# Kernel tuning notes

Measured on AMD Instinct MI355X. Metric: run time of the kernel, lower is better.

Reference implementation:

```python
import jax, jax.numpy as jnp
import numpy as np

HEAD_DIM = 64
HIDDEN_SIZE = 3072
NUM_HEADS = 48
B, TXT, VID = 1, 256, 1792
N = TXT + VID


def _layernorm(x, g, b, eps=1e-5):
    mu = jnp.mean(x, axis=-1, keepdims=True)
    xc = x - mu
    var = jnp.mean(xc * xc, axis=-1, keepdims=True)
    return xc * jax.lax.rsqrt(var + eps) * g + b


def _apply_rope1(x, freqs):
    # x: [B, L, H, D]; freqs: [1, 1, Lf, D//2, 2, 2]
    Bx, L, H, D = x.shape
    x_ = x.reshape(Bx, L, H, D // 2, 1, 2)
    # faithful to torch: if dim-2 sizes mismatch (H vs Lf), slice freqs to H
    if x_.shape[2] != 1 and freqs.shape[2] != 1 and x_.shape[2] != freqs.shape[2]:
        freqs = freqs[:, :, : x_.shape[2]]
    out = freqs[..., 0] * x_[..., 0] + freqs[..., 1] * x_[..., 1]
    return out.reshape(Bx, L, H, D).astype(x.dtype)


def setup_inputs() -> dict:
    key = jax.random.key(0)
    ks = jax.random.split(key, 16)
    s = 1.0 / np.sqrt(HIDDEN_SIZE)
    d = dict(
        combined=jax.random.normal(ks[0], (B, N, HIDDEN_SIZE), jnp.float32),
        freqs=jax.random.normal(ks[1], (1, 1, VID, HEAD_DIM // 2, 2, 2), jnp.float32),
        Wq=jax.random.normal(ks[2], (HIDDEN_SIZE, HIDDEN_SIZE), jnp.float32) * s,
        bq=jnp.zeros((HIDDEN_SIZE,), jnp.float32),
        Wk=jax.random.normal(ks[3], (HIDDEN_SIZE, HIDDEN_SIZE), jnp.float32) * s,
        bk=jnp.zeros((HIDDEN_SIZE,), jnp.float32),
        Wv=jax.random.normal(ks[4], (HIDDEN_SIZE, HIDDEN_SIZE), jnp.float32) * s,
        bv=jnp.zeros((HIDDEN_SIZE,), jnp.float32),
        Wo=jax.random.normal(ks[5], (HIDDEN_SIZE, HIDDEN_SIZE), jnp.float32) * s,
        bo=jnp.zeros((HIDDEN_SIZE,), jnp.float32),
        gq=jnp.ones((HEAD_DIM,), jnp.float32),
        bgq=jnp.zeros((HEAD_DIM,), jnp.float32),
        gk=jnp.ones((HEAD_DIM,), jnp.float32),
        bgk=jnp.zeros((HEAD_DIM,), jnp.float32),
        txt_len=TXT,
    )
    return d


def reference(combined, freqs, Wq, bq, Wk, bk, Wv, bv, Wo, bo, gq, bgq, gk, bgk, txt_len):
    Bx, Nx, _ = combined.shape
    Q = (combined @ Wq.T + bq).reshape(Bx, Nx, NUM_HEADS, HEAD_DIM)
    K = (combined @ Wk.T + bk).reshape(Bx, Nx, NUM_HEADS, HEAD_DIM)
    V = (combined @ Wv.T + bv).reshape(Bx, Nx, NUM_HEADS, HEAD_DIM)
    Q = _layernorm(Q, gq, bgq)
    K = _layernorm(K, gk, bgk)
    if freqs is not None and Nx - txt_len > 0:
        Q_vid = _apply_rope1(Q[:, txt_len:], freqs)
        K_vid = _apply_rope1(K[:, txt_len:], freqs)
        Q = jnp.concatenate([Q[:, :txt_len], Q_vid], axis=1)
        K = jnp.concatenate([K[:, :txt_len], K_vid], axis=1)
    # SDPA in fp32: [B, H, N, D]
    q = Q.transpose(0, 2, 1, 3).astype(jnp.float32)
    k = K.transpose(0, 2, 1, 3).astype(jnp.float32)
    v = V.transpose(0, 2, 1, 3).astype(jnp.float32)
    scale = 1.0 / np.sqrt(HEAD_DIM)
    scores = jnp.einsum('bhqd,bhkd->bhqk', q, k) * scale
    probs = jax.nn.softmax(scores, axis=-1)
    attn = jnp.einsum('bhqk,bhkd->bhqd', probs, v).astype(combined.dtype)
    attn = attn.transpose(0, 2, 1, 3).reshape(Bx, Nx, HIDDEN_SIZE)
    out = attn @ Wo.T + bo
    return out[:, txt_len:], out[:, :txt_len]
```

## Files before the change

kernel.cpp:

```cpp
#include <hip/hip_runtime.h>
#include <hip/hip_bf16.h>

typedef __attribute__((ext_vector_type(8))) short bf16x8;
typedef __attribute__((ext_vector_type(4))) float f32x4;
typedef unsigned int __attribute__((address_space(1))) as1_uint;
typedef unsigned int __attribute__((address_space(3))) as3_uint;

#define TXT 256
#define VIDN 1792
#define SEQ 2048
#define HID 3072
#define NH 48
#define HD 64
#define QSCALE 0.18033688011112042f

__device__ __forceinline__ unsigned short f2bf(float f) {
  union { float f; unsigned int u; } x; x.f = f;
  unsigned int r = x.u + 0x7fffu + ((x.u >> 16) & 1u);
  return (unsigned short)(r >> 16);
}

__device__ __forceinline__ void gload16(const void* g, void* l) {
  __builtin_amdgcn_global_load_lds((const as1_uint*)g, (as3_uint*)l, 16, 0, 0);
}

__global__ __launch_bounds__(256) void cvt_kernel(const float* __restrict__ s,
                                                  unsigned short* __restrict__ d, int n) {
  int i = (blockIdx.x * 256 + threadIdx.x) * 4;
  if (i >= n) return;
  float4 v = *(const float4*)(s + i);
  ushort4 o;
  o.x = f2bf(v.x); o.y = f2bf(v.y); o.z = f2bf(v.z); o.w = f2bf(v.w);
  *(ushort4*)(d + i) = o;
}

__global__ __launch_bounds__(256) void cvt3_kernel(const float* __restrict__ a,
                                                   const float* __restrict__ b,
                                                   const float* __restrict__ c,
                                                   unsigned short* __restrict__ d) {
  const int per = (HID * HID) / 1024;
  int bid = blockIdx.x;
  int m = bid / per, r = bid - m * per;
  const float* s = (m == 0) ? a : (m == 1) ? b : c;
  int i = (r * 256 + threadIdx.x) * 4;
  float4 v = *(const float4*)(s + i);
  ushort4 o;
  o.x = f2bf(v.x); o.y = f2bf(v.y); o.z = f2bf(v.z); o.w = f2bf(v.w);
  *(ushort4*)(d + (size_t)m * HID * HID + i) = o;
}

template<int MODE>
__global__ __launch_bounds__(512) void gemm256(
    const unsigned short* __restrict__ A,
    const unsigned short* __restrict__ Bt,
    int K, int ntn,
    float* __restrict__ Cq, unsigned short* __restrict__ Vt, const float* __restrict__ bv,
    float* __restrict__ Cout, const float* __restrict__ bo)
{
  __shared__ unsigned short lds[4 * 2 * 8192];
  const int tid = threadIdx.x;
  const int mt = blockIdx.x / ntn, nt = blockIdx.x % ntn;
  const int m0 = mt * 256, n0 = nt * 256;
  const int w = tid >> 6, lane = tid & 63, lr = lane & 15, lg = lane >> 4;
  const int wr = w >> 2, wc = w & 3;
  f32x4 acc[8][4] = {};
  const int NT = K >> 5;

#define STAGE(t)                                                               \
  {                                                                            \
    const int slot_ = (t) & 3;                                                 \
    const int k0_ = (t) << 5;                                                  \
    _Pragma("unroll")                                                          \
    for (int c = 0; c < 2; ++c) {                                              \
      int off = (c * 512 + tid) * 16;                                          \
      int row = off >> 6, cb = off & 63;                                       \
      gload16(A + (size_t)(m0 + row) * K + k0_ + (cb >> 1),                    \
              (char*)lds + slot_ * 32768 + off);                               \
      gload16(Bt + (size_t)(n0 + row) * K + k0_ + (cb >> 1),                   \
              (char*)lds + slot_ * 32768 + 16384 + off);                       \
    }                                                                          \
  }

#define COMPUTE(t)                                                             \
  {                                                                            \
    const unsigned short* lA = lds + ((t) & 3) * 16384;                        \
    const unsigned short* lB = lA + 8192;                                      \
    bf16x8 bfr[4];                                                             \
    _Pragma("unroll")                                                          \
    for (int nf = 0; nf < 4; ++nf)                                             \
      bfr[nf] = *(const bf16x8*)&lB[(wc * 64 + nf * 16 + lr) * 32 + lg * 8];   \
    __builtin_amdgcn_s_setprio(1);                                             \
    _Pragma("unroll")                                                          \
    for (int mf = 0; mf < 8; ++mf) {                                           \
      bf16x8 af = *(const bf16x8*)&lA[(wr * 128 + mf * 16 + lr) * 32 + lg * 8];\
      acc[mf][0] = __builtin_amdgcn_mfma_f32_16x16x32_bf16(af, bfr[0], acc[mf][0], 0, 0, 0); \
      acc[mf][1] = __builtin_amdgcn_mfma_f32_16x16x32_bf16(af, bfr[1], acc[mf][1], 0, 0, 0); \
      acc[mf][2] = __builtin_amdgcn_mfma_f32_16x16x32_bf16(af, bfr[2], acc[mf][2], 0, 0, 0); \
      acc[mf][3] = __builtin_amdgcn_mfma_f32_16x16x32_bf16(af, bfr[3], acc[mf][3], 0, 0, 0); \
    }                                                                          \
    __builtin_amdgcn_s_setprio(0);                                             \
  }

  STAGE(0); STAGE(1); STAGE(2);
  int t = 0;
  for (; t < NT - 3; ++t) {
    __builtin_amdgcn_s_barrier();
    STAGE(t + 3);
    asm volatile("s_waitcnt vmcnt(12)" ::: "memory");
    COMPUTE(t);
  }
  __builtin_amdgcn_s_barrier();
  asm volatile("s_waitcnt vmcnt(8)" ::: "memory");
  COMPUTE(t); ++t;
  __builtin_amdgcn_s_barrier();
  asm volatile("s_waitcnt vmcnt(4)" ::: "memory");
  COMPUTE(t); ++t;
  __builtin_amdgcn_s_barrier();
  asm volatile("s_waitcnt vmcnt(0)" ::: "memory");
  COMPUTE(t);
#undef STAGE
#undef COMPUTE

  if (MODE == 0) {
    if (n0 < 6144) {
#pragma unroll
      for (int mf = 0; mf < 8; ++mf) {
        int row = m0 + wr * 128 + mf * 16 + lg * 4;
#pragma unroll
        for (int nf = 0; nf < 4; ++nf) {
          int col = n0 + wc * 64 + nf * 16 + lr;
#pragma unroll
          for (int j = 0; j < 4; ++j)
            Cq[(size_t)(row + j) * 6144 + col] = acc[mf][nf][j];
        }
      }
    } else {
#pragma unroll
      for (int mf = 0; mf < 8; ++mf) {
        int srow = m0 + wr * 128 + mf * 16 + lg * 4;
#pragma unroll
        for (int nf = 0; nf < 4; ++nf) {
          int n2 = n0 - 6144 + wc * 64 + nf * 16 + lr;
          float b = bv[n2];
          ushort4 pk;
          pk.x = f2bf(acc[mf][nf][0] + b);
          pk.y = f2bf(acc[mf][nf][1] + b);
          pk.z = f2bf(acc[mf][nf][2] + b);
          pk.w = f2bf(acc[mf][nf][3] + b);
          *(ushort4*)(Vt + (size_t)n2 * SEQ + srow) = pk;
        }
      }
    }
  } else {
#pragma unroll
    for (int mf = 0; mf < 8; ++mf) {
      int row = m0 + wr * 128 + mf * 16 + lg * 4;
#pragma unroll
      for (int nf = 0; nf < 4; ++nf) {
        int col = n0 + wc * 64 + nf * 16 + lr;
        float b = bo[col];
#pragma unroll
        for (int j = 0; j < 4; ++j) {
          int s = row + j;
          int orow = (s >= TXT) ? (s - TXT) : (VIDN + s);
          Cout[(size_t)orow * HID + col] = acc[mf][nf][j] + b;
        }
      }
    }
  }
}

__global__ __launch_bounds__(256) void ln_rope_kernel(
    const float* __restrict__ QK,
    const float* __restrict__ bq, const float* __restrict__ bk,
    const float* __restrict__ gq, const float* __restrict__ bgq,
    const float* __restrict__ gk, const float* __restrict__ bgk,
    const float* __restrict__ freqs,
    unsigned short* __restrict__ Qh, unsigned short* __restrict__ Kh)
{
  int wid = blockIdx.x * 4 + (threadIdx.x >> 6);
  int lane = threadIdx.x & 63;
  int s = wid / 96;
  int rem = wid - s * 96;
  int h = rem >> 1, qk = rem & 1;
  int col = h * 64 + lane;
  float x = QK[(size_t)s * 6144 + qk * 3072 + col] + (qk ? bk[col] : bq[col]);
  float m = x;
#pragma unroll
  for (int msk = 1; msk < 64; msk <<= 1) m += __shfl_xor(m, msk);
  float mu = m * (1.0f / 64.0f);
  float xc = x - mu;
  float v = xc * xc;
#pragma unroll
  for (int msk = 1; msk < 64; msk <<= 1) v += __shfl_xor(v, msk);
  float rstd = rsqrtf(v * (1.0f / 64.0f) + 1e-5f);
  float y = xc * rstd * (qk ? gk[lane] : gq[lane]) + (qk ? bgk[lane] : bgq[lane]);
  if (s >= TXT) {
    float p = __shfl_xor(y, 1);
    float xe = (lane & 1) ? p : y;
    float xo = (lane & 1) ? y : p;
    int base = h * 128 + (lane >> 1) * 4 + (lane & 1) * 2;
    y = freqs[base] * xe + freqs[base + 1] * xo;
  }
  if (!qk) y *= QSCALE;
  (qk ? Kh : Qh)[((size_t)h * SEQ + s) * 64 + lane] = f2bf(y);
}

__global__ __launch_bounds__(512) void fattn_kernel(
    const unsigned short* __restrict__ Qh, const unsigned short* __restrict__ Kh,
    const unsigned short* __restrict__ Vt, unsigned short* __restrict__ ctx)
{
  __shared__ unsigned short kt[2][64][32];
  __shared__ unsigned short vt[2][64][32];
  __shared__ unsigned short pl[8][16][72];
  const int h = blockIdx.x >> 4;
  const int q0 = (blockIdx.x & 15) * 128;
  const int tid = threadIdx.x, w = tid >> 6, lane = tid & 63, lr = lane & 15, lg = lane >> 4;

  bf16x8 qf0, qf1;
  {
    const unsigned short* qp = Qh + ((size_t)h * SEQ + q0 + w * 16 + lr) * 64 + lg * 8;
    qf0 = *(const bf16x8*)qp;
    qf1 = *(const bf16x8*)(qp + 32);
  }
  f32x4 oacc[4] = {};
  float mrun = -1e30f, lrun = 0.f;

  for (int kv0 = 0; kv0 < SEQ; kv0 += 64) {
    __syncthreads();
    {
      int off = tid * 16;
      int half = off >> 12;
      int rem = off & 4095;
      int row = rem >> 6, cb = rem & 63;
      gload16(Kh + ((size_t)h * SEQ + kv0 + row) * 64 + half * 32 + (cb >> 1), (char*)kt + off);
      gload16(Vt + ((size_t)(h * 64 + row)) * SEQ + kv0 + half * 32 + (cb >> 1), (char*)vt + off);
    }
    __syncthreads();

    f32x4 sacc[4] = {};
    __builtin_amdgcn_s_setprio(1);
#pragma unroll
    for (int nf = 0; nf < 4; ++nf) {
      bf16x8 a0 = *(const bf16x8*)&kt[0][nf * 16 + lr][lg * 8];
      bf16x8 a1 = *(const bf16x8*)&kt[1][nf * 16 + lr][lg * 8];
      sacc[nf] = __builtin_amdgcn_mfma_f32_16x16x32_bf16(a0, qf0, sacc[nf], 0, 0, 0);
      sacc[nf] = __builtin_amdgcn_mfma_f32_16x16x32_bf16(a1, qf1, sacc[nf], 0, 0, 0);
    }
    __builtin_amdgcn_s_setprio(0);

    float mx;
    {
      float t0 = fmaxf(fmaxf(sacc[0][0], sacc[0][1]), fmaxf(sacc[0][2], sacc[0][3]));
      float t1 = fmaxf(fmaxf(sacc[1][0], sacc[1][1]), fmaxf(sacc[1][2], sacc[1][3]));
      float t2 = fmaxf(fmaxf(sacc[2][0], sacc[2][1]), fmaxf(sacc[2][2], sacc[2][3]));
      float t3 = fmaxf(fmaxf(sacc[3][0], sacc[3][1]), fmaxf(sacc[3][2], sacc[3][3]));
      mx = fmaxf(fmaxf(t0, t1), fmaxf(t2, t3));
    }
    mx = fmaxf(mx, __shfl_xor(mx, 16));
    mx = fmaxf(mx, __shfl_xor(mx, 32));

    if (!__all(mx <= mrun + 8.0f)) {
      float mn = fmaxf(mrun, mx);
      float corr = exp2f(mrun - mn);
      lrun *= corr;
      mrun = mn;
      float c0 = __shfl(corr, lg * 4 + 0);
      float c1 = __shfl(corr, lg * 4 + 1);
      float c2 = __shfl(corr, lg * 4 + 2);
      float c3 = __shfl(corr, lg * 4 + 3);
#pragma unroll
      for (int df = 0; df < 4; ++df) {
        oacc[df][0] *= c0; oacc[df][1] *= c1;
        oacc[df][2] *= c2; oacc[df][3] *= c3;
      }
    }

    float pr[4][4];
#pragma unroll
    for (int nf = 0; nf < 4; ++nf)
#pragma unroll
      for (int r = 0; r < 4; ++r)
        pr[nf][r] = exp2f(sacc[nf][r] - mrun);
    float rs;
    {
      float s0 = (pr[0][0] + pr[0][1]) + (pr[0][2] + pr[0][3]);
      float s1 = (pr[1][0] + pr[1][1]) + (pr[1][2] + pr[1][3]);
      float s2 = (pr[2][0] + pr[2][1]) + (pr[2][2] + pr[2][3]);
      float s3 = (pr[3][0] + pr[3][1]) + (pr[3][2] + pr[3][3]);
      rs = (s0 + s1) + (s2 + s3);
    }
    rs += __shfl_xor(rs, 16);
    rs += __shfl_xor(rs, 32);
    lrun += rs;

#pragma unroll
    for (int nf = 0; nf < 4; ++nf) {
      union { __hip_bfloat162 h; unsigned int u; } c0, c1;
      c0.h = __float22bfloat162_rn(make_float2(pr[nf][0], pr[nf][1]));
      c1.h = __float22bfloat162_rn(make_float2(pr[nf][2], pr[nf][3]));
      uint2 pw; pw.x = c0.u; pw.y = c1.u;
      *(uint2*)&pl[w][lr][nf * 16 + lg * 4] = pw;
    }

    bf16x8 pa0 = *(const bf16x8*)&pl[w][lr][lg * 8];
    bf16x8 pa1 = *(const bf16x8*)&pl[w][lr][32 + lg * 8];
    __builtin_amdgcn_s_setprio(1);
#pragma unroll
    for (int df = 0; df < 4; ++df) {
      bf16x8 v0 = *(const bf16x8*)&vt[0][df * 16 + lr][lg * 8];
      bf16x8 v1 = *(const bf16x8*)&vt[1][df * 16 + lr][lg * 8];
      oacc[df] = __builtin_amdgcn_mfma_f32_16x16x32_bf16(pa0, v0, oacc[df], 0, 0, 0);
      oacc[df] = __builtin_amdgcn_mfma_f32_16x16x32_bf16(pa1, v1, oacc[df], 0, 0, 0);
    }
    __builtin_amdgcn_s_setprio(0);
  }

  float linv = 1.0f / lrun;
  float i0 = __shfl(linv, lg * 4 + 0);
  float i1 = __shfl(linv, lg * 4 + 1);
  float i2 = __shfl(linv, lg * 4 + 2);
  float i3 = __shfl(linv, lg * 4 + 3);
#pragma unroll
  for (int df = 0; df < 4; ++df) {
    int s = q0 + w * 16 + lg * 4;
    int dcol = h * 64 + df * 16 + lr;
    ctx[(size_t)(s + 0) * HID + dcol] = f2bf(oacc[df][0] * i0);
    ctx[(size_t)(s + 1) * HID + dcol] = f2bf(oacc[df][1] * i1);
    ctx[(size_t)(s + 2) * HID + dcol] = f2bf(oacc[df][2] * i2);
    ctx[(size_t)(s + 3) * HID + dcol] = f2bf(oacc[df][3] * i3);
  }
}

extern "C" void kernel_launch(void* const* d_in, const int* in_sizes, int n_in,
                              void* d_out, int out_size, void* d_ws, size_t ws_size,
                              hipStream_t stream) {
  const float* combined = (const float*)d_in[0];
  const float* freqs    = (const float*)d_in[1];
  const float* Wq  = (const float*)d_in[2];
  const float* bq  = (const float*)d_in[3];
  const float* Wk  = (const float*)d_in[4];
  const float* bk  = (const float*)d_in[5];
  const float* Wv  = (const float*)d_in[6];
  const float* bv  = (const float*)d_in[7];
  const float* Wo  = (const float*)d_in[8];
  const float* bo  = (const float*)d_in[9];
  const float* gq  = (const float*)d_in[10];
  const float* bgq = (const float*)d_in[11];
  const float* gk  = (const float*)d_in[12];
  const float* bgk = (const float*)d_in[13];
  float* out = (float*)d_out;

  char* ws = (char*)d_ws;
  unsigned short* Abf  = (unsigned short*)ws; ws += (size_t)SEQ * HID * 2;
  unsigned short* Wqkv = (unsigned short*)ws; ws += (size_t)3 * HID * HID * 2;
  float*          QK   = (float*)ws;          ws += (size_t)SEQ * 6144 * 4;
  unsigned short* Qh   = (unsigned short*)ws; ws += (size_t)NH * SEQ * HD * 2;
  unsigned short* Kh   = (unsigned short*)ws; ws += (size_t)NH * SEQ * HD * 2;
  unsigned short* Vt   = (unsigned short*)ws; ws += (size_t)NH * HD * SEQ * 2;
  unsigned short* Wob  = (unsigned short*)QK;
  unsigned short* ctx  = Abf;

  cvt_kernel<<<(SEQ * HID) / 1024, 256, 0, stream>>>(combined, Abf, SEQ * HID);
  cvt3_kernel<<<3 * (HID * HID) / 1024, 256, 0, stream>>>(Wq, Wk, Wv, Wqkv);

  gemm256<0><<<8 * 36, 512, 0, stream>>>(Abf, Wqkv, HID, 36, QK, Vt, bv, nullptr, nullptr);

  ln_rope_kernel<<<(SEQ * NH * 2) / 4, 256, 0, stream>>>(QK, bq, bk, gq, bgq, gk, bgk, freqs, Qh, Kh);

  cvt_kernel<<<(HID * HID) / 1024, 256, 0, stream>>>(Wo, Wob, HID * HID);

  fattn_kernel<<<NH * 16, 512, 0, stream>>>(Qh, Kh, Vt, ctx);

  gemm256<1><<<8 * 12, 512, 0, stream>>>(ctx, Wob, HID, 12, nullptr, nullptr, nullptr, out, bo);
}
```

Baseline: 453.7 us.

## Shrink GEMM M-tile to 128 and use 3-stage LDS pipeline for more blocks

Measured after the change: 430.2 us. 5.2% less time.

```diff
diff --git a/kernel.cpp b/kernel.cpp
--- a/kernel.cpp
+++ b/kernel.cpp
@@ -22,6 +22,12 @@
 
 __device__ __forceinline__ void gload16(const void* g, void* l) {
   __builtin_amdgcn_global_load_lds((const as1_uint*)g, (as3_uint*)l, 16, 0, 0);
+}
+
+__device__ __forceinline__ void fbar() {
+  asm volatile("" ::: "memory");
+  __builtin_amdgcn_s_barrier();
+  asm volatile("" ::: "memory");
 }
 
 __global__ __launch_bounds__(256) void cvt_kernel(const float* __restrict__ s,
@@ -50,49 +56,53 @@
 }
 
 template<int MODE>
-__global__ __launch_bounds__(512) void gemm256(
+__global__ __launch_bounds__(512, 4) void gemm256(
     const unsigned short* __restrict__ A,
     const unsigned short* __restrict__ Bt,
     int K, int ntn,
     float* __restrict__ Cq, unsigned short* __restrict__ Vt, const float* __restrict__ bv,
     float* __restrict__ Cout, const float* __restrict__ bo)
 {
-  __shared__ unsigned short lds[4 * 2 * 8192];
+  __shared__ unsigned short lds[3 * 12288];
   const int tid = threadIdx.x;
   const int mt = blockIdx.x / ntn, nt = blockIdx.x % ntn;
-  const int m0 = mt * 256, n0 = nt * 256;
+  const int m0 = mt * 128, n0 = nt * 256;
   const int w = tid >> 6, lane = tid & 63, lr = lane & 15, lg = lane >> 4;
   const int wr = w >> 2, wc = w & 3;
-  f32x4 acc[8][4] = {};
+  f32x4 acc[4][4] = {};
   const int NT = K >> 5;
 
 #define STAGE(t)                                                               \
   {                                                                            \
-    const int slot_ = (t) & 3;                                                 \
+    const int slot_ = (t) % 3;                                                 \
     const int k0_ = (t) << 5;                                                  \
+    char* base_ = (char*)lds + slot_ * 24576;                                  \
+    {                                                                          \
+      int off = tid * 16;                                                      \
+      int row = off >> 6, cb = off & 63;                                       \
+      gload16(A + (size_t)(m0 + row) * K + k0_ + (cb >> 1), base_ + off);      \
+    }                                                                          \
     _Pragma("unroll")                                                          \
     for (int c = 0; c < 2; ++c) {                                              \
       int off = (c * 512 + tid) * 16;                                          \
       int row = off >> 6, cb = off & 63;                                       \
-      gload16(A + (size_t)(m0 + row) * K + k0_ + (cb >> 1),                    \
-              (char*)lds + slot_ * 32768 + off);                               \
       gload16(Bt + (size_t)(n0 + row) * K + k0_ + (cb >> 1),                   \
-              (char*)lds + slot_ * 32768 + 16384 + off);                       \
+              base_ + 8192 + off);                                             \
     }                                                                          \
   }
 
 #define COMPUTE(t)                                                             \
   {                                                                            \
-    const unsigned short* lA = lds + ((t) & 3) * 16384;                        \
-    const unsigned short* lB = lA + 8192;                                      \
+    const unsigned short* lA = lds + ((t) % 3) * 12288;                        \
+    const unsigned short* lB = lA + 4096;                                      \
     bf16x8 bfr[4];                                                             \
     _Pragma("unroll")                                                          \
     for (int nf = 0; nf < 4; ++nf)                                             \
       bfr[nf] = *(const bf16x8*)&lB[(wc * 64 + nf * 16 + lr) * 32 + lg * 8];   \
     __builtin_amdgcn_s_setprio(1);                                             \
     _Pragma("unroll")                                                          \
-    for (int mf = 0; mf < 8; ++mf) {                                           \
-      bf16x8 af = *(const bf16x8*)&lA[(wr * 128 + mf * 16 + lr) * 32 + lg * 8];\
+    for (int mf = 0; mf < 4; ++mf) {                                           \
+      bf16x8 af = *(const bf16x8*)&lA[(wr * 64 + mf * 16 + lr) * 32 + lg * 8]; \
       acc[mf][0] = __builtin_amdgcn_mfma_f32_16x16x32_bf16(af, bfr[0], acc[mf][0], 0, 0, 0); \
       acc[mf][1] = __builtin_amdgcn_mfma_f32_16x16x32_bf16(af, bfr[1], acc[mf][1], 0, 0, 0); \
       acc[mf][2] = __builtin_amdgcn_mfma_f32_16x16x32_bf16(af, bfr[2], acc[mf][2], 0, 0, 0); \
@@ -101,22 +111,21 @@
     __builtin_amdgcn_s_setprio(0);                                             \
   }
 
-  STAGE(0); STAGE(1); STAGE(2);
+  STAGE(0); STAGE(1);
   int t = 0;
-  for (; t < NT - 3; ++t) {
-    __builtin_amdgcn_s_barrier();
-    STAGE(t + 3);
-    asm volatile("s_waitcnt vmcnt(12)" ::: "memory");
+  for (; t < NT - 2; ++t) {
+    STAGE(t + 2);
+    asm volatile("s_waitcnt vmcnt(6)" ::: "memory");
+    fbar();
     COMPUTE(t);
-  }
-  __builtin_amdgcn_s_barrier();
-  asm volatile("s_waitcnt vmcnt(8)" ::: "memory");
+    fbar();
+  }
+  asm volatile("s_waitcnt vmcnt(3)" ::: "memory");
+  fbar();
   COMPUTE(t); ++t;
-  __builtin_amdgcn_s_barrier();
-  asm volatile("s_waitcnt vmcnt(4)" ::: "memory");
-  COMPUTE(t); ++t;
-  __builtin_amdgcn_s_barrier();
+  fbar();
   asm volatile("s_waitcnt vmcnt(0)" ::: "memory");
+  fbar();
   COMPUTE(t);
 #undef STAGE
 #undef COMPUTE
@@ -124,8 +133,8 @@
   if (MODE == 0) {
     if (n0 < 6144) {
 #pragma unroll
-      for (int mf = 0; mf < 8; ++mf) {
-        int row = m0 + wr * 128 + mf * 16 + lg * 4;
+      for (int mf = 0; mf < 4; ++mf) {
+        int row = m0 + wr * 64 + mf * 16 + lg * 4;
 #pragma unroll
         for (int nf = 0; nf < 4; ++nf) {
           int col = n0 + wc * 64 + nf * 16 + lr;
@@ -136,8 +145,8 @@
       }
     } else {
 #pragma unroll
-      for (int mf = 0; mf < 8; ++mf) {
-        int srow = m0 + wr * 128 + mf * 16 + lg * 4;
+      for (int mf = 0; mf < 4; ++mf) {
+        int srow = m0 + wr * 64 + mf * 16 + lg * 4;
 #pragma unroll
         for (int nf = 0; nf < 4; ++nf) {
           int n2 = n0 - 6144 + wc * 64 + nf * 16 + lr;
@@ -153,8 +162,8 @@
     }
   } else {
 #pragma unroll
-    for (int mf = 0; mf < 8; ++mf) {
-      int row = m0 + wr * 128 + mf * 16 + lg * 4;
+    for (int mf = 0; mf < 4; ++mf) {
+      int row = m0 + wr * 64 + mf * 16 + lg * 4;
 #pragma unroll
       for (int nf = 0; nf < 4; ++nf) {
         int col = n0 + wc * 64 + nf * 16 + lr;
@@ -364,7 +373,7 @@
   cvt_kernel<<<(SEQ * HID) / 1024, 256, 0, stream>>>(combined, Abf, SEQ * HID);
   cvt3_kernel<<<3 * (HID * HID) / 1024, 256, 0, stream>>>(Wq, Wk, Wv, Wqkv);
 
-  gemm256<0><<<8 * 36, 512, 0, stream>>>(Abf, Wqkv, HID, 36, QK, Vt, bv, nullptr, nullptr);
+  gemm256<0><<<16 * 36, 512, 0, stream>>>(Abf, Wqkv, HID, 36, QK, Vt, bv, nullptr, nullptr);
 
   ln_rope_kernel<<<(SEQ * NH * 2) / 4, 256, 0, stream>>>(QK, bq, bk, gq, bgq, gk, bgk, freqs, Qh, Kh);
 
@@ -372,5 +381,5 @@
 
   fattn_kernel<<<NH * 16, 512, 0, stream>>>(Qh, Kh, Vt, ctx);
 
-  gemm256<1><<<8 * 12, 512, 0, stream>>>(ctx, Wob, HID, 12, nullptr, nullptr, nullptr, out, bo);
-}
+  gemm256<1><<<16 * 12, 512, 0, stream>>>(ctx, Wob, HID, 12, nullptr, nullptr, nullptr, out, bo);
+}
```
